# Kernel tuning notes

Measured on AMD Instinct MI355X. Metric: run time of the kernel, lower is better.

Reference implementation:

```python
import jax, jax.numpy as jnp
import numpy as np

EPS = 1e-3  # Keras BatchNormalization default epsilon

def _bn(x, g, b, m, v):
    return (x - m) * (g / jnp.sqrt(v + EPS)) + b

def _conv1d(x, w, b):
    # x: [B,T,Cin], w: [K,Cin,Cout], VALID padding
    y = jax.lax.conv_general_dilated(x, w, window_strides=(1,), padding='VALID',
                                     dimension_numbers=('NWC', 'WIO', 'NWC'))
    return y + b

def _lstm(x, W, U, b, return_sequences):
    # Keras LSTM: gates order [i, f, c, o]; sigmoid recurrent act, tanh act
    B, T, _ = x.shape
    H = U.shape[0]
    xz = jnp.einsum('btf,fh->bth', x, W) + b  # precompute input projection [B,T,4H]
    def step(carry, xz_t):
        h, c = carry
        z = xz_t + h @ U
        i, f, g, o = jnp.split(z, 4, axis=-1)
        i = jax.nn.sigmoid(i); f = jax.nn.sigmoid(f)
        g = jnp.tanh(g);       o = jax.nn.sigmoid(o)
        c = f * c + i * g
        h = o * jnp.tanh(c)
        return (h, c), h
    h0 = jnp.zeros((B, H), x.dtype)
    (h_last, _), hs = jax.lax.scan(step, (h0, h0), jnp.swapaxes(xz, 0, 1))
    return jnp.swapaxes(hs, 0, 1) if return_sequences else h_last

def setup_inputs() -> dict:
    key = jax.random.key(0)
    ks = jax.random.split(key, 32)
    B, T, F, C = 4096, 512, 10, 5
    s = 0.1
    d = {}
    d['x'] = jax.random.normal(ks[0], (B, T, F), jnp.float32)
    def bn(i, ch, p):
        d[p + '_g'] = jnp.ones((ch,), jnp.float32) + s * jax.random.normal(ks[i], (ch,))
        d[p + '_b'] = s * jax.random.normal(ks[i + 1], (ch,))
        d[p + '_m'] = s * jax.random.normal(ks[i + 2], (ch,))
        d[p + '_v'] = jnp.ones((ch,), jnp.float32) + 0.05 * jax.random.uniform(ks[i + 3], (ch,))
    bn(1, F, 'bn1'); bn(5, 16, 'bn2'); bn(9, 32, 'bn3')
    d['conv1_w'] = s * jax.random.normal(ks[13], (3, F, 16), jnp.float32)
    d['conv1_b'] = s * jax.random.normal(ks[14], (16,), jnp.float32)
    d['conv2_w'] = s * jax.random.normal(ks[15], (6, 16, 32), jnp.float32)
    d['conv2_b'] = s * jax.random.normal(ks[16], (32,), jnp.float32)
    def lstm_p(i, fin, h, p):
        d[p + '_W'] = s * jax.random.normal(ks[i], (fin, 4 * h), jnp.float32)
        d[p + '_U'] = s * jax.random.normal(ks[i + 1], (h, 4 * h), jnp.float32)
        d[p + '_b'] = s * jax.random.normal(ks[i + 2], (4 * h,), jnp.float32)
    lstm_p(17, 32, 32, 'l1'); lstm_p(20, 32, 24, 'l2'); lstm_p(23, 24, 16, 'l3')
    d['d1_w'] = s * jax.random.normal(ks[26], (16, 8), jnp.float32)
    d['d1_b'] = s * jax.random.normal(ks[27], (8,), jnp.float32)
    d['out_w'] = s * jax.random.normal(ks[28], (8, C), jnp.float32)
    d['out_b'] = s * jax.random.normal(ks[29], (C,), jnp.float32)
    return d

def reference(x, bn1_g, bn1_b, bn1_m, bn1_v, conv1_w, conv1_b,
              bn2_g, bn2_b, bn2_m, bn2_v, conv2_w, conv2_b,
              bn3_g, bn3_b, bn3_m, bn3_v,
              l1_W, l1_U, l1_b, l2_W, l2_U, l2_b, l3_W, l3_U, l3_b,
              d1_w, d1_b, out_w, out_b):
    # inference mode (training=False): BN uses moving stats, dropout is identity
    h = _bn(x, bn1_g, bn1_b, bn1_m, bn1_v)
    h = jax.nn.relu(_conv1d(h, conv1_w, conv1_b))
    h = _bn(h, bn2_g, bn2_b, bn2_m, bn2_v)
    h = jax.nn.relu(_conv1d(h, conv2_w, conv2_b))
    h = _bn(h, bn3_g, bn3_b, bn3_m, bn3_v)
    h = _lstm(h, l1_W, l1_U, l1_b, True)
    h = _lstm(h, l2_W, l2_U, l2_b, True)
    h = _lstm(h, l3_W, l3_U, l3_b, False)  # [B,16]
    h = jax.nn.relu(h @ d1_w + d1_b)
    return jax.nn.softmax(h @ out_w + out_b, axis=-1)
```

## Files before the change

kernel.cpp:

```cpp
#include <hip/hip_runtime.h>
#include <math.h>

#define EPSBN 1e-3f

typedef unsigned long long ull;
typedef __attribute__((ext_vector_type(8))) short bf16x8;
typedef __attribute__((ext_vector_type(4))) float f32x4;

#define WS_W1F 0
#define WS_B1F 480
#define WS_B2F 496
#define WS_W2F 528
#define WS_BL1 3600
#define WS_BL2 3728
#define WS_BL3 3824
#define WS_B1P 3888
#define WS_B2P 7984
#define WS_B3P 11056
#define WS_R2  13104

__device__ __forceinline__ unsigned short f2b(float f) {
  unsigned u = __float_as_uint(f);
  return (unsigned short)((u + 0x7FFFu + ((u >> 16) & 1u)) >> 16);
}
__device__ __forceinline__ float sigm(float v) { return 1.f / (1.f + __expf(-v)); }
__device__ __forceinline__ float tanh_(float v) {
  float e = __expf(-2.f * fabsf(v));
  float t = (1.f - e) / (1.f + e);
  return copysignf(t, v);
}
__device__ __forceinline__ float gate_h(const float* __restrict__ z, int H, int u, float& c) {
  float gi = sigm(z[u]), gf = sigm(z[H + u]), gg = tanh_(z[2 * H + u]), go = sigm(z[3 * H + u]);
  c = fmaf(gf, c, gi * gg);
  return go * tanh_(c);
}

__global__ __launch_bounds__(256) void prep_kernel(
    const float* __restrict__ bn1g, const float* __restrict__ bn1b,
    const float* __restrict__ bn1m, const float* __restrict__ bn1v,
    const float* __restrict__ bn2g, const float* __restrict__ bn2b,
    const float* __restrict__ bn2m, const float* __restrict__ bn2v,
    const float* __restrict__ bn3g, const float* __restrict__ bn3b,
    const float* __restrict__ bn3m, const float* __restrict__ bn3v,
    const float* __restrict__ c1w, const float* __restrict__ c1b,
    const float* __restrict__ c2w, const float* __restrict__ c2b,
    const float* __restrict__ l1W, const float* __restrict__ l1U, const float* __restrict__ l1b,
    const float* __restrict__ l2W, const float* __restrict__ l2U, const float* __restrict__ l2b,
    const float* __restrict__ l3W, const float* __restrict__ l3U, const float* __restrict__ l3b,
    float* __restrict__ ws)
{
  __shared__ float s1[10], t1[10], s2[16], t2[16], s3[32], t3[32];
  int tid = threadIdx.x;
  if (tid < 10)                  { float s = bn1g[tid] * rsqrtf(bn1v[tid] + EPSBN); s1[tid] = s; t1[tid] = bn1b[tid] - bn1m[tid] * s; }
  else if (tid >= 32 && tid < 48){ int c = tid - 32; float s = bn2g[c] * rsqrtf(bn2v[c] + EPSBN); s2[c] = s; t2[c] = bn2b[c] - bn2m[c] * s; }
  else if (tid >= 64 && tid < 96){ int c = tid - 64; float s = bn3g[c] * rsqrtf(bn3v[c] + EPSBN); s3[c] = s; t3[c] = bn3b[c] - bn3m[c] * s; }
  __syncthreads();

  float* w1f = ws + WS_W1F;
  float* b1f = ws + WS_B1F;
  float* b2f = ws + WS_B2F;
  float* w2f = ws + WS_W2F;
  float* bL1 = ws + WS_BL1;
  float* bL2 = ws + WS_BL2;
  float* bL3 = ws + WS_BL3;
  unsigned short* B1P = (unsigned short*)(ws + WS_B1P);
  unsigned short* B2P = (unsigned short*)(ws + WS_B2P);
  unsigned short* B3P = (unsigned short*)(ws + WS_B3P);

  for (int i = tid; i < 480; i += 256) { int ci = (i >> 4) % 10; w1f[i] = c1w[i] * s1[ci]; }
  for (int co = tid; co < 16; co += 256) {
    float a = c1b[co];
    for (int k = 0; k < 3; k++) for (int ci = 0; ci < 10; ci++) a += t1[ci] * c1w[(k * 10 + ci) * 16 + co];
    b1f[co] = a;
  }
  for (int i = tid; i < 3072; i += 256) { int ci = (i >> 5) & 15; w2f[i] = c2w[i] * s2[ci]; }
  for (int co = tid; co < 32; co += 256) {
    float a = c2b[co];
    for (int k = 0; k < 6; k++) for (int ci = 0; ci < 16; ci++) a += t2[ci] * c2w[(k * 16 + ci) * 32 + co];
    b2f[co] = a;
  }
  for (int j = tid; j < 128; j += 256) {
    float a = l1b[j];
    for (int k = 0; k < 32; k++) a += t3[k] * l1W[k * 128 + j];
    bL1[j] = a;
  }
  for (int j = tid; j < 96; j += 256) bL2[j] = l2b[j];
  for (int j = tid; j < 64; j += 256) bL3[j] = l3b[j];

  for (int i = tid; i < 2 * 8 * 64 * 8; i += 256) {
    int e = i & 7, l = (i >> 3) & 63, nt = (i >> 9) & 7, kt = i >> 12;
    int j = nt * 16 + (l & 15);
    int k = kt * 32 + ((l >> 4) << 3) + e;
    float v = (k < 32) ? l1W[k * 128 + j] * s3[k] : l1U[(k - 32) * 128 + j];
    B1P[i] = f2b(v);
  }
  for (int i = tid; i < 2 * 6 * 64 * 8; i += 256) {
    int e = i & 7, l = (i >> 3) & 63, m = i >> 9;
    int nt = m % 6, kt = m / 6;
    int j = nt * 16 + (l & 15);
    int k = kt * 32 + ((l >> 4) << 3) + e;
    float v = (k < 32) ? l2W[k * 96 + j] : ((k < 56) ? l2U[(k - 32) * 96 + j] : 0.f);
    B2P[i] = f2b(v);
  }
  for (int i = tid; i < 2 * 4 * 64 * 8; i += 256) {
    int e = i & 7, l = (i >> 3) & 63, m = i >> 9;
    int nt = m & 3, kt = m >> 2;
    int j = nt * 16 + (l & 15);
    int k = kt * 32 + ((l >> 4) << 3) + e;
    float v = (k < 24) ? l3W[k * 64 + j] : ((k < 40) ? l3U[(k - 24) * 64 + j] : 0.f);
    B3P[i] = f2b(v);
  }
}

#define CT 128
__global__ __launch_bounds__(256, 4) void conv_kernel(
    const float* __restrict__ x, const float* __restrict__ ws,
    unsigned short* __restrict__ r2, int row0)
{
  int b  = row0 + blockIdx.y;
  int bl = blockIdx.y;
  int t0 = blockIdx.x * CT;
  int n2 = min(CT, 505 - t0);
  int n1 = n2 + 5;
  int nx = n1 + 2;
  int tid = threadIdx.x;

  __shared__ float xs[135 * 10];
  __shared__ float r1s[133 * 17];
  __shared__ float w1f[480];
  __shared__ float b1f[16];
  alignas(16) __shared__ float w2f[3072];
  __shared__ float b2f[32];

  for (int i = tid; i < 480;  i += 256) w1f[i] = ws[WS_W1F + i];
  for (int i = tid; i < 16;   i += 256) b1f[i] = ws[WS_B1F + i];
  for (int i = tid; i < 32;   i += 256) b2f[i] = ws[WS_B2F + i];
  for (int i = tid; i < 3072; i += 256) w2f[i] = ws[WS_W2F + i];
  const float* xb = x + (size_t)b * 512 * 10 + (size_t)t0 * 10;
  for (int i = tid; i < nx * 10; i += 256) xs[i] = xb[i];
  __syncthreads();

  #pragma unroll 1
  for (int i = tid; i < n1 * 16; i += 256) {
    int tt = i >> 4, c = i & 15;
    float a = b1f[c];
    #pragma unroll
    for (int k = 0; k < 3; k++)
      #pragma unroll
      for (int ci = 0; ci < 10; ci++)
        a = fmaf(xs[(tt + k) * 10 + ci], w1f[(k * 10 + ci) * 16 + c], a);
    r1s[tt * 17 + c] = fmaxf(a, 0.f);
  }
  __syncthreads();

  int cog = (tid & 7) * 4;
  int tg  = (tid >> 3) * 4;
  float acc[4][4];
  #pragma unroll
  for (int i2 = 0; i2 < 4; i2++)
    #pragma unroll
    for (int j2 = 0; j2 < 4; j2++) acc[i2][j2] = b2f[cog + j2];
  #pragma unroll 4
  for (int kc = 0; kc < 96; kc++) {
    int k2 = kc >> 4;
    float4 w4 = *(const float4*)&w2f[kc * 32 + cog];
    #pragma unroll
    for (int i2 = 0; i2 < 4; i2++) {
      float xv = r1s[(tg + i2 + k2) * 17 + (kc & 15)];
      acc[i2][0] = fmaf(xv, w4.x, acc[i2][0]);
      acc[i2][1] = fmaf(xv, w4.y, acc[i2][1]);
      acc[i2][2] = fmaf(xv, w4.z, acc[i2][2]);
      acc[i2][3] = fmaf(xv, w4.w, acc[i2][3]);
    }
  }
  #pragma unroll
  for (int i2 = 0; i2 < 4; i2++) {
    int tt = tg + i2;
    if (tt < n2) {
      ull o = (ull)f2b(fmaxf(acc[i2][0], 0.f))
            | ((ull)f2b(fmaxf(acc[i2][1], 0.f)) << 16)
            | ((ull)f2b(fmaxf(acc[i2][2], 0.f)) << 32)
            | ((ull)f2b(fmaxf(acc[i2][3], 0.f)) << 48);
      *(ull*)&r2[((size_t)bl * 505 + (t0 + tt)) * 32 + cog] = o;
    }
  }
}

#define SWZB(row, byte) ((byte) ^ (((row) & 7) << 4))
#define MFMA(a, b, c) __builtin_amdgcn_mfma_f32_16x16x32_bf16((a), (b), (c), 0, 0, 0)
#define ZST1 132
#define ZST2 100
#define ZST3 68

__global__ __launch_bounds__(256, 4) void lstm_kernel(
    const unsigned short* __restrict__ r2, const float* __restrict__ ws,
    const float* __restrict__ d1w, const float* __restrict__ d1b,
    const float* __restrict__ outw, const float* __restrict__ outb,
    float* __restrict__ out, int row0)
{
  int tid = threadIdx.x;
  int l   = tid & 63;
  int w   = tid >> 6;
  int r16 = l & 15;
  int g   = l >> 4;
  int rl  = blockIdx.x * 4;

  alignas(16) __shared__ unsigned short xh1[16 * 64];
  alignas(16) __shared__ unsigned short xh2[16 * 64];
  alignas(16) __shared__ unsigned short xh3[16 * 64];
  __shared__ float zb1[4 * ZST1];
  __shared__ float zb2[4 * ZST2];
  __shared__ float zb3[4 * ZST3];
  __shared__ float hstash[4 * 16];

  const unsigned short* B1P = (const unsigned short*)(ws + WS_B1P);
  const unsigned short* B2P = (const unsigned short*)(ws + WS_B2P);
  const unsigned short* B3P = (const unsigned short*)(ws + WS_B3P);

  const unsigned short* Bp; const float* bbase; const unsigned short* xs8;
  float* zw; int zst, NJ, jo, ntt;
  if (w == 0)      { Bp = B1P; bbase = ws + WS_BL1; xs8 = xh1; zw = zb1; zst = ZST1; NJ = 4; jo = 0; ntt = 8; }
  else if (w == 1) { Bp = B1P; bbase = ws + WS_BL1; xs8 = xh1; zw = zb1; zst = ZST1; NJ = 4; jo = 4; ntt = 8; }
  else if (w == 2) { Bp = B2P; bbase = ws + WS_BL2; xs8 = xh2; zw = zb2; zst = ZST2; NJ = 6; jo = 0; ntt = 6; }
  else             { Bp = B3P; bbase = ws + WS_BL3; xs8 = xh3; zw = zb3; zst = ZST3; NJ = 4; jo = 0; ntt = 4; }

  bf16x8 Bfr[12];
  float barr[6];
  #pragma unroll
  for (int j = 0; j < 6; j++) {
    if (j < NJ) {
      Bfr[2 * j]     = *(const bf16x8*)&Bp[((0 * ntt + jo + j) * 64 + l) * 8];
      Bfr[2 * j + 1] = *(const bf16x8*)&Bp[((1 * ntt + jo + j) * 64 + l) * 8];
      barr[j] = bbase[(jo + j) * 16 + r16];
    } else {
      barr[j] = 0.f;
      Bfr[2 * j] = (bf16x8)0; Bfr[2 * j + 1] = (bf16x8)0;
    }
  }

  float cA = 0.f, cB = 0.f;
  ull xreg = 0;
  const unsigned short* xp = nullptr;
  int xrow = 0, xch = 0;
  if (tid >= 224) {
    int slot = tid - 224;
    xrow = slot >> 3; xch = slot & 7;
    xp = r2 + ((size_t)(rl + xrow) * 505) * 32 + xch * 4;
    xreg = *(const ull*)xp;
  }

  for (int i = tid; i < 16 * 64; i += 256) { xh1[i] = 0; xh2[i] = 0; xh3[i] = 0; }
  if (tid < 64) hstash[tid] = 0.f;
  __syncthreads();
  if (tid >= 224) {
    *(ull*)((char*)xh1 + SWZB(xrow, xrow * 128 + xch * 8)) = xreg;
    xreg = *(const ull*)(xp + 32);
  }
  __syncthreads();

  #pragma unroll 1
  for (int i = 0; i < 507; ++i) {
    {
      bf16x8 a0 = *(const bf16x8*)((const char*)xs8 + SWZB(r16, r16 * 128 + g * 16));
      bf16x8 a1 = *(const bf16x8*)((const char*)xs8 + SWZB(r16, r16 * 128 + 64 + g * 16));
      #pragma unroll
      for (int j = 0; j < 6; j++) {
        if (j < NJ) {
          f32x4 ac = {barr[j], barr[j], barr[j], barr[j]};
          ac = MFMA(a0, Bfr[2 * j], ac);
          ac = MFMA(a1, Bfr[2 * j + 1], ac);
          if (g == 0) {
            int c = (jo + j) * 16 + r16;
            #pragma unroll
            for (int q = 0; q < 4; q++) zw[q * zst + c] = ac[q];
          }
        }
      }
    }
    __syncthreads();
    if (w < 2) {
      if (i <= 504) {
        int s = tid, r = s >> 5, u = s & 31;
        float h = gate_h(zb1 + r * ZST1, 32, u, cA);
        unsigned short hb = f2b(h);
        *(unsigned short*)((char*)xh1 + SWZB(r, r * 128 + (32 + u) * 2)) = hb;
        *(unsigned short*)((char*)xh2 + SWZB(r, r * 128 + u * 2)) = hb;
      }
    } else if (w == 2) {
      if (i >= 1 && i <= 505) {
        int s = tid - 128;
        int r = s / 24, u = s - r * 24;
        float h = gate_h(zb2 + r * ZST2, 24, u, cA);
        unsigned short hb = f2b(h);
        *(unsigned short*)((char*)xh2 + SWZB(r, r * 128 + (32 + u) * 2)) = hb;
        *(unsigned short*)((char*)xh3 + SWZB(r, r * 128 + u * 2)) = hb;
        if (tid < 160) {
          int s2 = tid - 128 + 64;
          int rB = s2 / 24, uB = s2 - rB * 24;
          float hB = gate_h(zb2 + rB * ZST2, 24, uB, cB);
          unsigned short hbB = f2b(hB);
          *(unsigned short*)((char*)xh2 + SWZB(rB, rB * 128 + (32 + uB) * 2)) = hbB;
          *(unsigned short*)((char*)xh3 + SWZB(rB, rB * 128 + uB * 2)) = hbB;
        }
      }
    } else {
      if (i >= 2) {
        int s = tid - 192, r = s >> 4, u = s & 15;
        float h = gate_h(zb3 + r * ZST3, 16, u, cA);
        *(unsigned short*)((char*)xh3 + SWZB(r, r * 128 + (24 + u) * 2)) = f2b(h);
        hstash[r * 16 + u] = h;
      }
      if (tid >= 224) {
        if (i < 504) *(ull*)((char*)xh1 + SWZB(xrow, xrow * 128 + xch * 8)) = xreg;
        if (i < 503) xreg = *(const ull*)(xp + (size_t)(i + 2) * 32);
      }
    }
    __syncthreads();
  }

  if (tid < 4) {
    int row = tid;
    float hd[16];
    #pragma unroll
    for (int u = 0; u < 16; u++) hd[u] = hstash[row * 16 + u];
    float aa[8];
    #pragma unroll
    for (int o = 0; o < 8; o++) {
      float acc = d1b[o];
      #pragma unroll
      for (int u = 0; u < 16; u++) acc = fmaf(hd[u], d1w[u * 8 + o], acc);
      aa[o] = fmaxf(acc, 0.f);
    }
    float oo[5]; float mx = -1e30f;
    #pragma unroll
    for (int cc = 0; cc < 5; cc++) {
      float acc = outb[cc];
      #pragma unroll
      for (int o = 0; o < 8; o++) acc = fmaf(aa[o], outw[o * 5 + cc], acc);
      oo[cc] = acc; mx = fmaxf(mx, acc);
    }
    float sum = 0.f;
    #pragma unroll
    for (int cc = 0; cc < 5; cc++) { oo[cc] = __expf(oo[cc] - mx); sum += oo[cc]; }
    float inv = 1.f / sum;
    #pragma unroll
    for (int cc = 0; cc < 5; cc++) out[(size_t)(row0 + rl + row) * 5 + cc] = oo[cc] * inv;
  }
}

extern "C" void kernel_launch(void* const* d_in, const int* in_sizes, int n_in,
                              void* d_out, int out_size, void* d_ws, size_t ws_size,
                              hipStream_t stream)
{
  const float* x    = (const float*)d_in[0];
  const float* bn1g = (const float*)d_in[1];
  const float* bn1b = (const float*)d_in[2];
  const float* bn1m = (const float*)d_in[3];
  const float* bn1v = (const float*)d_in[4];
  const float* bn2g = (const float*)d_in[5];
  const float* bn2b = (const float*)d_in[6];
  const float* bn2m = (const float*)d_in[7];
  const float* bn2v = (const float*)d_in[8];
  const float* bn3g = (const float*)d_in[9];
  const float* bn3b = (const float*)d_in[10];
  const float* bn3m = (const float*)d_in[11];
  const float* bn3v = (const float*)d_in[12];
  const float* c1w  = (const float*)d_in[13];
  const float* c1b  = (const float*)d_in[14];
  const float* c2w  = (const float*)d_in[15];
  const float* c2b  = (const float*)d_in[16];
  const float* l1W  = (const float*)d_in[17];
  const float* l1U  = (const float*)d_in[18];
  const float* l1b  = (const float*)d_in[19];
  const float* l2W  = (const float*)d_in[20];
  const float* l2U  = (const float*)d_in[21];
  const float* l2b  = (const float*)d_in[22];
  const float* l3W  = (const float*)d_in[23];
  const float* l3U  = (const float*)d_in[24];
  const float* l3b  = (const float*)d_in[25];
  const float* d1w  = (const float*)d_in[26];
  const float* d1b  = (const float*)d_in[27];
  const float* outw = (const float*)d_in[28];
  const float* outb = (const float*)d_in[29];

  float* ws = (float*)d_ws;
  unsigned short* r2 = (unsigned short*)(ws + WS_R2);

  prep_kernel<<<1, 256, 0, stream>>>(bn1g, bn1b, bn1m, bn1v,
                                     bn2g, bn2b, bn2m, bn2v,
                                     bn3g, bn3b, bn3m, bn3v,
                                     c1w, c1b, c2w, c2b,
                                     l1W, l1U, l1b, l2W, l2U, l2b, l3W, l3U, l3b,
                                     ws);

  size_t availB = (ws_size > (size_t)WS_R2 * 4) ? ws_size - (size_t)WS_R2 * 4 : 0;
  int nch = 1;
  while ((size_t)(4096 / nch) * 505 * 32 * 2 > availB && nch < 16) nch <<= 1;
  int rows_pc = 4096 / nch;

  for (int ch = 0; ch < nch; ++ch) {
    int row0 = ch * rows_pc;
    dim3 cgrid(4, rows_pc);
    conv_kernel<<<cgrid, 256, 0, stream>>>(x, ws, r2, row0);
    lstm_kernel<<<rows_pc / 4, 256, 0, stream>>>(r2, ws, d1w, d1b, outw, outb, (float*)d_out, row0);
  }
}
```

Before: 1.088 ms.

## Double-buffer LSTM state and fuse gate math into MFMA lanes, one barrier per step

The LSTM kernel now double-buffers the bf16 x/h tiles so each timestep needs a single barrier instead of two. Layers 1 and 3 compute their gate nonlinearities directly from the MFMA accumulators, using weights permuted so that each wave holds all four gates for its units, which avoids staging through shared memory. Sigmoid and tanh switch to rcp-based approximations, and the conv kernel processes 4 batch rows per block to amortize its weight loads. The costs are more shared memory, fewer active lanes doing gate math, and slightly lower numeric precision.

```diff
diff --git a/kernel.cpp b/kernel.cpp
--- a/kernel.cpp
+++ b/kernel.cpp
@@ -4,6 +4,7 @@
 #define EPSBN 1e-3f
 
 typedef unsigned long long ull;
+typedef unsigned short u16;
 typedef __attribute__((ext_vector_type(8))) short bf16x8;
 typedef __attribute__((ext_vector_type(4))) float f32x4;
 
@@ -19,21 +20,12 @@
 #define WS_B3P 11056
 #define WS_R2  13104
 
-__device__ __forceinline__ unsigned short f2b(float f) {
+__device__ __forceinline__ u16 f2b(float f) {
   unsigned u = __float_as_uint(f);
-  return (unsigned short)((u + 0x7FFFu + ((u >> 16) & 1u)) >> 16);
+  return (u16)((u + 0x7FFFu + ((u >> 16) & 1u)) >> 16);
 }
-__device__ __forceinline__ float sigm(float v) { return 1.f / (1.f + __expf(-v)); }
-__device__ __forceinline__ float tanh_(float v) {
-  float e = __expf(-2.f * fabsf(v));
-  float t = (1.f - e) / (1.f + e);
-  return copysignf(t, v);
-}
-__device__ __forceinline__ float gate_h(const float* __restrict__ z, int H, int u, float& c) {
-  float gi = sigm(z[u]), gf = sigm(z[H + u]), gg = tanh_(z[2 * H + u]), go = sigm(z[3 * H + u]);
-  c = fmaf(gf, c, gi * gg);
-  return go * tanh_(c);
-}
+__device__ __forceinline__ float sigm(float v)  { return __builtin_amdgcn_rcpf(1.f + __expf(-v)); }
+__device__ __forceinline__ float tanh_(float v) { return fmaf(2.f, __builtin_amdgcn_rcpf(1.f + __expf(-2.f * v)), -1.f); }
 
 __global__ __launch_bounds__(256) void prep_kernel(
     const float* __restrict__ bn1g, const float* __restrict__ bn1b,
@@ -63,9 +55,9 @@
   float* bL1 = ws + WS_BL1;
   float* bL2 = ws + WS_BL2;
   float* bL3 = ws + WS_BL3;
-  unsigned short* B1P = (unsigned short*)(ws + WS_B1P);
-  unsigned short* B2P = (unsigned short*)(ws + WS_B2P);
-  unsigned short* B3P = (unsigned short*)(ws + WS_B3P);
+  u16* B1P = (u16*)(ws + WS_B1P);
+  u16* B2P = (u16*)(ws + WS_B2P);
+  u16* B3P = (u16*)(ws + WS_B3P);
 
   for (int i = tid; i < 480; i += 256) { int ci = (i >> 4) % 10; w1f[i] = c1w[i] * s1[ci]; }
   for (int co = tid; co < 16; co += 256) {
@@ -89,7 +81,8 @@
 
   for (int i = tid; i < 2 * 8 * 64 * 8; i += 256) {
     int e = i & 7, l = (i >> 3) & 63, nt = (i >> 9) & 7, kt = i >> 12;
-    int j = nt * 16 + (l & 15);
+    int g = nt & 3, uh = nt >> 2;
+    int j = g * 32 + uh * 16 + (l & 15);
     int k = kt * 32 + ((l >> 4) << 3) + e;
     float v = (k < 32) ? l1W[k * 128 + j] * s3[k] : l1U[(k - 32) * 128 + j];
     B1P[i] = f2b(v);
@@ -115,10 +108,8 @@
 #define CT 128
 __global__ __launch_bounds__(256, 4) void conv_kernel(
     const float* __restrict__ x, const float* __restrict__ ws,
-    unsigned short* __restrict__ r2, int row0)
+    u16* __restrict__ r2, int row0)
 {
-  int b  = row0 + blockIdx.y;
-  int bl = blockIdx.y;
   int t0 = blockIdx.x * CT;
   int n2 = min(CT, 505 - t0);
   int n1 = n2 + 5;
@@ -136,64 +127,67 @@
   for (int i = tid; i < 16;   i += 256) b1f[i] = ws[WS_B1F + i];
   for (int i = tid; i < 32;   i += 256) b2f[i] = ws[WS_B2F + i];
   for (int i = tid; i < 3072; i += 256) w2f[i] = ws[WS_W2F + i];
-  const float* xb = x + (size_t)b * 512 * 10 + (size_t)t0 * 10;
-  for (int i = tid; i < nx * 10; i += 256) xs[i] = xb[i];
-  __syncthreads();
-
-  #pragma unroll 1
-  for (int i = tid; i < n1 * 16; i += 256) {
-    int tt = i >> 4, c = i & 15;
-    float a = b1f[c];
-    #pragma unroll
-    for (int k = 0; k < 3; k++)
-      #pragma unroll
-      for (int ci = 0; ci < 10; ci++)
-        a = fmaf(xs[(tt + k) * 10 + ci], w1f[(k * 10 + ci) * 16 + c], a);
-    r1s[tt * 17 + c] = fmaxf(a, 0.f);
-  }
-  __syncthreads();
 
   int cog = (tid & 7) * 4;
   int tg  = (tid >> 3) * 4;
-  float acc[4][4];
-  #pragma unroll
-  for (int i2 = 0; i2 < 4; i2++)
-    #pragma unroll
-    for (int j2 = 0; j2 < 4; j2++) acc[i2][j2] = b2f[cog + j2];
-  #pragma unroll 4
-  for (int kc = 0; kc < 96; kc++) {
-    int k2 = kc >> 4;
-    float4 w4 = *(const float4*)&w2f[kc * 32 + cog];
+
+  for (int rr = 0; rr < 4; rr++) {
+    int bl = blockIdx.y * 4 + rr;
+    __syncthreads();
+    const float* xb = x + ((size_t)(row0 + bl) * 512 + t0) * 10;
+    for (int i = tid; i < nx * 10; i += 256) xs[i] = xb[i];
+    __syncthreads();
+
+    #pragma unroll 1
+    for (int i = tid; i < n1 * 16; i += 256) {
+      int tt = i >> 4, c = i & 15;
+      float a = b1f[c];
+      #pragma unroll
+      for (int k = 0; k < 3; k++)
+        #pragma unroll
+        for (int ci = 0; ci < 10; ci++)
+          a = fmaf(xs[(tt + k) * 10 + ci], w1f[(k * 10 + ci) * 16 + c], a);
+      r1s[tt * 17 + c] = fmaxf(a, 0.f);
+    }
+    __syncthreads();
+
+    float acc[4][4];
+    #pragma unroll
+    for (int i2 = 0; i2 < 4; i2++)
+      #pragma unroll
+      for (int j2 = 0; j2 < 4; j2++) acc[i2][j2] = b2f[cog + j2];
+    #pragma unroll 4
+    for (int kc = 0; kc < 96; kc++) {
+      int k2 = kc >> 4;
+      float4 w4 = *(const float4*)&w2f[kc * 32 + cog];
+      #pragma unroll
+      for (int i2 = 0; i2 < 4; i2++) {
+        float xv = r1s[(tg + i2 + k2) * 17 + (kc & 15)];
+        acc[i2][0] = fmaf(xv, w4.x, acc[i2][0]);
+        acc[i2][1] = fmaf(xv, w4.y, acc[i2][1]);
+        acc[i2][2] = fmaf(xv, w4.z, acc[i2][2]);
+        acc[i2][3] = fmaf(xv, w4.w, acc[i2][3]);
+      }
+    }
     #pragma unroll
     for (int i2 = 0; i2 < 4; i2++) {
-      float xv = r1s[(tg + i2 + k2) * 17 + (kc & 15)];
-      acc[i2][0] = fmaf(xv, w4.x, acc[i2][0]);
-      acc[i2][1] = fmaf(xv, w4.y, acc[i2][1]);
-      acc[i2][2] = fmaf(xv, w4.z, acc[i2][2]);
-      acc[i2][3] = fmaf(xv, w4.w, acc[i2][3]);
-    }
-  }
-  #pragma unroll
-  for (int i2 = 0; i2 < 4; i2++) {
-    int tt = tg + i2;
-    if (tt < n2) {
-      ull o = (ull)f2b(fmaxf(acc[i2][0], 0.f))
-            | ((ull)f2b(fmaxf(acc[i2][1], 0.f)) << 16)
-            | ((ull)f2b(fmaxf(acc[i2][2], 0.f)) << 32)
-            | ((ull)f2b(fmaxf(acc[i2][3], 0.f)) << 48);
-      *(ull*)&r2[((size_t)bl * 505 + (t0 + tt)) * 32 + cog] = o;
+      int tt = tg + i2;
+      if (tt < n2) {
+        ull o = (ull)f2b(fmaxf(acc[i2][0], 0.f))
+              | ((ull)f2b(fmaxf(acc[i2][1], 0.f)) << 16)
+              | ((ull)f2b(fmaxf(acc[i2][2], 0.f)) << 32)
+              | ((ull)f2b(fmaxf(acc[i2][3], 0.f)) << 48);
+        *(ull*)&r2[((size_t)bl * 505 + (t0 + tt)) * 32 + cog] = o;
+      }
     }
   }
 }
 
-#define SWZB(row, byte) ((byte) ^ (((row) & 7) << 4))
+#define SWZ(row, byte) ((byte) ^ (((row) & 7) << 4))
 #define MFMA(a, b, c) __builtin_amdgcn_mfma_f32_16x16x32_bf16((a), (b), (c), 0, 0, 0)
-#define ZST1 132
-#define ZST2 100
-#define ZST3 68
-
-__global__ __launch_bounds__(256, 4) void lstm_kernel(
-    const unsigned short* __restrict__ r2, const float* __restrict__ ws,
+
+__global__ __launch_bounds__(256, 5) void lstm_kernel(
+    const u16* __restrict__ r2, const float* __restrict__ ws,
     const float* __restrict__ d1w, const float* __restrict__ d1b,
     const float* __restrict__ outw, const float* __restrict__ outb,
     float* __restrict__ out, int row0)
@@ -205,114 +199,168 @@
   int g   = l >> 4;
   int rl  = blockIdx.x * 4;
 
-  alignas(16) __shared__ unsigned short xh1[16 * 64];
-  alignas(16) __shared__ unsigned short xh2[16 * 64];
-  alignas(16) __shared__ unsigned short xh3[16 * 64];
-  __shared__ float zb1[4 * ZST1];
-  __shared__ float zb2[4 * ZST2];
-  __shared__ float zb3[4 * ZST3];
+  alignas(16) __shared__ u16 xh1[2][16 * 64];
+  alignas(16) __shared__ u16 xh2[2][16 * 64];
+  alignas(16) __shared__ u16 xh3[2][16 * 64];
+  alignas(16) __shared__ float zb[96 * 4];
   __shared__ float hstash[4 * 16];
 
-  const unsigned short* B1P = (const unsigned short*)(ws + WS_B1P);
-  const unsigned short* B2P = (const unsigned short*)(ws + WS_B2P);
-  const unsigned short* B3P = (const unsigned short*)(ws + WS_B3P);
-
-  const unsigned short* Bp; const float* bbase; const unsigned short* xs8;
-  float* zw; int zst, NJ, jo, ntt;
-  if (w == 0)      { Bp = B1P; bbase = ws + WS_BL1; xs8 = xh1; zw = zb1; zst = ZST1; NJ = 4; jo = 0; ntt = 8; }
-  else if (w == 1) { Bp = B1P; bbase = ws + WS_BL1; xs8 = xh1; zw = zb1; zst = ZST1; NJ = 4; jo = 4; ntt = 8; }
-  else if (w == 2) { Bp = B2P; bbase = ws + WS_BL2; xs8 = xh2; zw = zb2; zst = ZST2; NJ = 6; jo = 0; ntt = 6; }
-  else             { Bp = B3P; bbase = ws + WS_BL3; xs8 = xh3; zw = zb3; zst = ZST3; NJ = 4; jo = 0; ntt = 4; }
-
-  bf16x8 Bfr[12];
-  float barr[6];
-  #pragma unroll
-  for (int j = 0; j < 6; j++) {
-    if (j < NJ) {
-      Bfr[2 * j]     = *(const bf16x8*)&Bp[((0 * ntt + jo + j) * 64 + l) * 8];
-      Bfr[2 * j + 1] = *(const bf16x8*)&Bp[((1 * ntt + jo + j) * 64 + l) * 8];
-      barr[j] = bbase[(jo + j) * 16 + r16];
-    } else {
-      barr[j] = 0.f;
-      Bfr[2 * j] = (bf16x8)0; Bfr[2 * j + 1] = (bf16x8)0;
-    }
-  }
-
-  float cA = 0.f, cB = 0.f;
+  const u16* B1P = (const u16*)(ws + WS_B1P);
+  const u16* B2P = (const u16*)(ws + WS_B2P);
+  const u16* B3P = (const u16*)(ws + WS_B3P);
+
+  bf16x8 F[6][2];
+  float bias[6];
+  if (w < 2) {
+    #pragma unroll
+    for (int g4 = 0; g4 < 4; g4++) {
+      F[g4][0] = *(const bf16x8*)&B1P[((0 * 8 + w * 4 + g4) * 64 + l) * 8];
+      F[g4][1] = *(const bf16x8*)&B1P[((1 * 8 + w * 4 + g4) * 64 + l) * 8];
+      bias[g4] = ws[WS_BL1 + g4 * 32 + w * 16 + r16];
+    }
+    bias[4] = bias[5] = 0.f; F[4][0] = F[4][1] = F[5][0] = F[5][1] = (bf16x8)0;
+  } else if (w == 2) {
+    #pragma unroll
+    for (int j = 0; j < 6; j++) {
+      F[j][0] = *(const bf16x8*)&B2P[((0 * 6 + j) * 64 + l) * 8];
+      F[j][1] = *(const bf16x8*)&B2P[((1 * 6 + j) * 64 + l) * 8];
+      bias[j] = ws[WS_BL2 + j * 16 + r16];
+    }
+  } else {
+    #pragma unroll
+    for (int g4 = 0; g4 < 4; g4++) {
+      F[g4][0] = *(const bf16x8*)&B3P[((0 * 4 + g4) * 64 + l) * 8];
+      F[g4][1] = *(const bf16x8*)&B3P[((1 * 4 + g4) * 64 + l) * 8];
+      bias[g4] = ws[WS_BL3 + g4 * 16 + r16];
+    }
+    bias[4] = bias[5] = 0.f; F[4][0] = F[4][1] = F[5][0] = F[5][1] = (bf16x8)0;
+  }
+
+  float cA[4] = {0.f, 0.f, 0.f, 0.f};
+  float c2A = 0.f, c2B = 0.f;
+  int tid2 = tid - 128;
+  int r2A = tid2 / 24, u2A = tid2 - r2A * 24;
+  int s2B = tid2 + 64, r2B = s2B / 24, u2B = s2B - r2B * 24;
+
+  bool stager = (w == 3 && l >= 16 && l < 48);
+  int slot = l - 16;
+  int xrow = slot >> 3, xch = slot & 7;
+  const u16* xp = r2 + ((size_t)(rl + xrow) * 505) * 32 + xch * 4;
   ull xreg = 0;
-  const unsigned short* xp = nullptr;
-  int xrow = 0, xch = 0;
-  if (tid >= 224) {
-    int slot = tid - 224;
-    xrow = slot >> 3; xch = slot & 7;
-    xp = r2 + ((size_t)(rl + xrow) * 505) * 32 + xch * 4;
-    xreg = *(const ull*)xp;
-  }
-
-  for (int i = tid; i < 16 * 64; i += 256) { xh1[i] = 0; xh2[i] = 0; xh3[i] = 0; }
-  if (tid < 64) hstash[tid] = 0.f;
+
+  for (int i = tid; i < 16 * 64; i += 256) {
+    xh1[0][i] = 0; xh1[1][i] = 0; xh2[0][i] = 0; xh2[1][i] = 0; xh3[0][i] = 0; xh3[1][i] = 0;
+  }
   __syncthreads();
-  if (tid >= 224) {
-    *(ull*)((char*)xh1 + SWZB(xrow, xrow * 128 + xch * 8)) = xreg;
+  if (stager) {
+    ull x0 = *(const ull*)xp;
+    *(ull*)((char*)xh1[0] + SWZ(xrow, xrow * 128 + xch * 8)) = x0;
     xreg = *(const ull*)(xp + 32);
   }
   __syncthreads();
 
   #pragma unroll 1
   for (int i = 0; i < 507; ++i) {
-    {
-      bf16x8 a0 = *(const bf16x8*)((const char*)xs8 + SWZB(r16, r16 * 128 + g * 16));
-      bf16x8 a1 = *(const bf16x8*)((const char*)xs8 + SWZB(r16, r16 * 128 + 64 + g * 16));
-      #pragma unroll
-      for (int j = 0; j < 6; j++) {
-        if (j < NJ) {
-          f32x4 ac = {barr[j], barr[j], barr[j], barr[j]};
-          ac = MFMA(a0, Bfr[2 * j], ac);
-          ac = MFMA(a1, Bfr[2 * j + 1], ac);
-          if (g == 0) {
-            int c = (jo + j) * 16 + r16;
-            #pragma unroll
-            for (int q = 0; q < 4; q++) zw[q * zst + c] = ac[q];
-          }
-        }
-      }
-    }
-    __syncthreads();
+    int p = i & 1;
+    u16* x1n = xh1[p ^ 1]; u16* x2n = xh2[p ^ 1]; u16* x3n = xh3[p ^ 1];
+
     if (w < 2) {
-      if (i <= 504) {
-        int s = tid, r = s >> 5, u = s & 31;
-        float h = gate_h(zb1 + r * ZST1, 32, u, cA);
-        unsigned short hb = f2b(h);
-        *(unsigned short*)((char*)xh1 + SWZB(r, r * 128 + (32 + u) * 2)) = hb;
-        *(unsigned short*)((char*)xh2 + SWZB(r, r * 128 + u * 2)) = hb;
+      const char* xc = (const char*)xh1[p];
+      bf16x8 A0 = *(const bf16x8*)(xc + SWZ(r16, r16 * 128 + g * 16));
+      bf16x8 A1 = *(const bf16x8*)(xc + SWZ(r16, r16 * 128 + 64 + g * 16));
+      f32x4 z0 = {bias[0], bias[0], bias[0], bias[0]};
+      f32x4 z1 = {bias[1], bias[1], bias[1], bias[1]};
+      f32x4 z2 = {bias[2], bias[2], bias[2], bias[2]};
+      f32x4 z3 = {bias[3], bias[3], bias[3], bias[3]};
+      z0 = MFMA(A0, F[0][0], z0); z0 = MFMA(A1, F[0][1], z0);
+      z1 = MFMA(A0, F[1][0], z1); z1 = MFMA(A1, F[1][1], z1);
+      z2 = MFMA(A0, F[2][0], z2); z2 = MFMA(A1, F[2][1], z2);
+      z3 = MFMA(A0, F[3][0], z3); z3 = MFMA(A1, F[3][1], z3);
+      if (g == 0 && i <= 504) {
+        int u = w * 16 + r16;
+        #pragma unroll
+        for (int q = 0; q < 4; q++) {
+          float gi = sigm(z0[q]), gf = sigm(z1[q]), gG = tanh_(z2[q]), go = sigm(z3[q]);
+          cA[q] = fmaf(gf, cA[q], gi * gG);
+          u16 hb = f2b(go * tanh_(cA[q]));
+          *(u16*)((char*)x1n + SWZ(q, q * 128 + (32 + u) * 2)) = hb;
+          *(u16*)((char*)x2n + SWZ(q, q * 128 + u * 2)) = hb;
+        }
       }
     } else if (w == 2) {
+      const char* xc = (const char*)xh2[p];
+      bf16x8 A0 = *(const bf16x8*)(xc + SWZ(r16, r16 * 128 + g * 16));
+      bf16x8 A1 = *(const bf16x8*)(xc + SWZ(r16, r16 * 128 + 64 + g * 16));
+      {
+        f32x4 za = {bias[0], bias[0], bias[0], bias[0]};
+        f32x4 zbv = {bias[1], bias[1], bias[1], bias[1]};
+        f32x4 zc = {bias[2], bias[2], bias[2], bias[2]};
+        za  = MFMA(A0, F[0][0], za);  za  = MFMA(A1, F[0][1], za);
+        zbv = MFMA(A0, F[1][0], zbv); zbv = MFMA(A1, F[1][1], zbv);
+        zc  = MFMA(A0, F[2][0], zc);  zc  = MFMA(A1, F[2][1], zc);
+        if (g == 0) {
+          *(f32x4*)&zb[(0 * 16 + r16) * 4] = za;
+          *(f32x4*)&zb[(1 * 16 + r16) * 4] = zbv;
+          *(f32x4*)&zb[(2 * 16 + r16) * 4] = zc;
+        }
+        za  = {bias[3], bias[3], bias[3], bias[3]};
+        zbv = {bias[4], bias[4], bias[4], bias[4]};
+        zc  = {bias[5], bias[5], bias[5], bias[5]};
+        za  = MFMA(A0, F[3][0], za);  za  = MFMA(A1, F[3][1], za);
+        zbv = MFMA(A0, F[4][0], zbv); zbv = MFMA(A1, F[4][1], zbv);
+        zc  = MFMA(A0, F[5][0], zc);  zc  = MFMA(A1, F[5][1], zc);
+        if (g == 0) {
+          *(f32x4*)&zb[(3 * 16 + r16) * 4] = za;
+          *(f32x4*)&zb[(4 * 16 + r16) * 4] = zbv;
+          *(f32x4*)&zb[(5 * 16 + r16) * 4] = zc;
+        }
+      }
       if (i >= 1 && i <= 505) {
-        int s = tid - 128;
-        int r = s / 24, u = s - r * 24;
-        float h = gate_h(zb2 + r * ZST2, 24, u, cA);
-        unsigned short hb = f2b(h);
-        *(unsigned short*)((char*)xh2 + SWZB(r, r * 128 + (32 + u) * 2)) = hb;
-        *(unsigned short*)((char*)xh3 + SWZB(r, r * 128 + u * 2)) = hb;
-        if (tid < 160) {
-          int s2 = tid - 128 + 64;
-          int rB = s2 / 24, uB = s2 - rB * 24;
-          float hB = gate_h(zb2 + rB * ZST2, 24, uB, cB);
-          unsigned short hbB = f2b(hB);
-          *(unsigned short*)((char*)xh2 + SWZB(rB, rB * 128 + (32 + uB) * 2)) = hbB;
-          *(unsigned short*)((char*)xh3 + SWZB(rB, rB * 128 + uB * 2)) = hbB;
+        {
+          float zi = zb[(u2A) * 4 + r2A], zf = zb[(24 + u2A) * 4 + r2A];
+          float zg = zb[(48 + u2A) * 4 + r2A], zo = zb[(72 + u2A) * 4 + r2A];
+          float gi = sigm(zi), gf = sigm(zf), gG = tanh_(zg), go = sigm(zo);
+          c2A = fmaf(gf, c2A, gi * gG);
+          u16 hb = f2b(go * tanh_(c2A));
+          *(u16*)((char*)x2n + SWZ(r2A, r2A * 128 + (32 + u2A) * 2)) = hb;
+          *(u16*)((char*)x3n + SWZ(r2A, r2A * 128 + u2A * 2)) = hb;
+        }
+        if (tid2 < 32) {
+          float zi = zb[(u2B) * 4 + r2B], zf = zb[(24 + u2B) * 4 + r2B];
+          float zg = zb[(48 + u2B) * 4 + r2B], zo = zb[(72 + u2B) * 4 + r2B];
+          float gi = sigm(zi), gf = sigm(zf), gG = tanh_(zg), go = sigm(zo);
+          c2B = fmaf(gf, c2B, gi * gG);
+          u16 hb = f2b(go * tanh_(c2B));
+          *(u16*)((char*)x2n + SWZ(r2B, r2B * 128 + (32 + u2B) * 2)) = hb;
+          *(u16*)((char*)x3n + SWZ(r2B, r2B * 128 + u2B * 2)) = hb;
         }
       }
     } else {
-      if (i >= 2) {
-        int s = tid - 192, r = s >> 4, u = s & 15;
-        float h = gate_h(zb3 + r * ZST3, 16, u, cA);
-        *(unsigned short*)((char*)xh3 + SWZB(r, r * 128 + (24 + u) * 2)) = f2b(h);
-        hstash[r * 16 + u] = h;
-      }
-      if (tid >= 224) {
-        if (i < 504) *(ull*)((char*)xh1 + SWZB(xrow, xrow * 128 + xch * 8)) = xreg;
-        if (i < 503) xreg = *(const ull*)(xp + (size_t)(i + 2) * 32);
+      const char* xc = (const char*)xh3[p];
+      bf16x8 A0 = *(const bf16x8*)(xc + SWZ(r16, r16 * 128 + g * 16));
+      bf16x8 A1 = *(const bf16x8*)(xc + SWZ(r16, r16 * 128 + 64 + g * 16));
+      f32x4 z0 = {bias[0], bias[0], bias[0], bias[0]};
+      f32x4 z1 = {bias[1], bias[1], bias[1], bias[1]};
+      f32x4 z2 = {bias[2], bias[2], bias[2], bias[2]};
+      f32x4 z3 = {bias[3], bias[3], bias[3], bias[3]};
+      z0 = MFMA(A0, F[0][0], z0); z0 = MFMA(A1, F[0][1], z0);
+      z1 = MFMA(A0, F[1][0], z1); z1 = MFMA(A1, F[1][1], z1);
+      z2 = MFMA(A0, F[2][0], z2); z2 = MFMA(A1, F[2][1], z2);
+      z3 = MFMA(A0, F[3][0], z3); z3 = MFMA(A1, F[3][1], z3);
+      if (g == 0 && i >= 2) {
+        int u = r16;
+        #pragma unroll
+        for (int q = 0; q < 4; q++) {
+          float gi = sigm(z0[q]), gf = sigm(z1[q]), gG = tanh_(z2[q]), go = sigm(z3[q]);
+          cA[q] = fmaf(gf, cA[q], gi * gG);
+          float h = go * tanh_(cA[q]);
+          *(u16*)((char*)x3n + SWZ(q, q * 128 + (24 + u) * 2)) = f2b(h);
+          if (i == 506) hstash[q * 16 + u] = h;
+        }
+      }
+      if (stager) {
+        *(ull*)((char*)x1n + SWZ(xrow, xrow * 128 + xch * 8)) = xreg;
+        if (i + 2 <= 504) xreg = *(const ull*)(xp + (size_t)(i + 2) * 32);
       }
     }
     __syncthreads();
@@ -384,7 +432,7 @@
   const float* outb = (const float*)d_in[29];
 
   float* ws = (float*)d_ws;
-  unsigned short* r2 = (unsigned short*)(ws + WS_R2);
+  u16* r2 = (u16*)(ws + WS_R2);
 
   prep_kernel<<<1, 256, 0, stream>>>(bn1g, bn1b, bn1m, bn1v,
                                      bn2g, bn2b, bn2m, bn2v,
@@ -400,7 +448,7 @@
 
   for (int ch = 0; ch < nch; ++ch) {
     int row0 = ch * rows_pc;
-    dim3 cgrid(4, rows_pc);
+    dim3 cgrid(4, rows_pc / 4);
     conv_kernel<<<cgrid, 256, 0, stream>>>(x, ws, r2, row0);
     lstm_kernel<<<rows_pc / 4, 256, 0, stream>>>(r2, ws, d1w, d1b, outw, outb, (float*)d_out, row0);
   }
```

Result: slower. 1.301 ms (+19.6%).
